# Kernel optimization log

Hardware: AMD Instinct MI355X
Metric: run time of the kernel (lower is better)

The kernel has to match this reference:

```python
import jax, jax.numpy as jnp
import numpy as np

B, P, M = 16, 16384, 2048
D_Z, D_PHI, D_R = 512, 256, 64
H1, H2 = 96, 96
IN_DIM = D_Z + 3 * D_PHI + D_R  # 1344


def setup_inputs() -> dict:
    key = jax.random.key(0)
    ks = jax.random.split(key, 8)
    g_q = jax.random.normal(ks[0], (B, D_Z), dtype=jnp.float32)
    Phi = jax.random.normal(ks[1], (M, D_PHI), dtype=jnp.float32)
    # pair indices with i < j (sort each row)
    pi = jax.random.randint(ks[2], (P, 2), 0, M, dtype=jnp.int64)
    pair_index = jnp.sort(pi, axis=-1)
    relation_features = jax.random.normal(ks[3], (P, D_R), dtype=jnp.float32)
    # learned MLP params (Linear weights stored [in, out])
    W1 = jax.random.normal(ks[4], (IN_DIM, H1), dtype=jnp.float32) / np.sqrt(IN_DIM)
    b1 = jnp.zeros((H1,), dtype=jnp.float32)
    W2 = jax.random.normal(ks[5], (H1, H2), dtype=jnp.float32) / np.sqrt(H1)
    b2 = jnp.zeros((H2,), dtype=jnp.float32)
    W3 = jax.random.normal(ks[6], (H2, 1), dtype=jnp.float32) / np.sqrt(H2)
    b3 = jnp.zeros((1,), dtype=jnp.float32)
    return {"g_q": g_q, "Phi": Phi, "pair_index": pair_index,
            "relation_features": relation_features,
            "W1": W1, "b1": b1, "W2": W2, "b2": b2, "W3": W3, "b3": b3}


def reference(g_q, Phi, pair_index, relation_features, W1, b1, W2, b2, W3, b3):
    # gather pair embeddings: [P, d_phi]
    phi_i = Phi[pair_index[:, 0]]
    phi_j = Phi[pair_index[:, 1]]
    # symmetric combine -> [P, 3*d_phi + d_r]
    pair_feats = jnp.concatenate(
        [phi_i + phi_j, jnp.abs(phi_i - phi_j), phi_i * phi_j, relation_features],
        axis=-1)
    b, p = g_q.shape[0], pair_feats.shape[0]
    # broadcast-concat -> x: [B, P, in_dim]
    x = jnp.concatenate(
        [jnp.broadcast_to(g_q[:, None, :], (b, p, g_q.shape[-1])),
         jnp.broadcast_to(pair_feats[None, :, :], (b, p, pair_feats.shape[-1]))],
        axis=-1)
    # small MLP: Linear -> GELU (erf, dropout is identity at eval) x2, then Linear(->1)
    h = jax.nn.gelu(x @ W1 + b1, approximate=False)
    h = jax.nn.gelu(h @ W2 + b2, approximate=False)
    out = h @ W3 + b3  # [B, P, 1]
    return out[..., 0]  # [B, P]
```

## Files before the change

### kernel.cpp

```cpp
#include <hip/hip_runtime.h>
#include <hip/hip_bf16.h>
#include <stdint.h>

static constexpr int P_N   = 16384;
static constexpr int D_Z   = 512;
static constexpr int D_PHI = 256;
static constexpr int D_R   = 64;
static constexpr int H     = 96;
static constexpr int KP    = 832;

using f32x4 = __attribute__((ext_vector_type(4))) float;
using s16x8 = __attribute__((ext_vector_type(8))) short;

__device__ __forceinline__ unsigned short f2bf(float f) {
    union { float f; uint32_t u; } v; v.f = f;
    return (unsigned short)((v.u + 0x7FFFu + ((v.u >> 16) & 1u)) >> 16);
}

__device__ __forceinline__ uint32_t pkbf2(float lo, float hi) {
    union { __hip_bfloat162 h; uint32_t u; } c;
    c.h = __float22bfloat162_rn(make_float2(lo, hi));
    return c.u;
}

__device__ __forceinline__ float gelu_f(float x) {
    float x2 = x * x;
    float u  = __builtin_fmaf(-0.1029444f, x2, -2.3022126f);
    float e  = __builtin_amdgcn_exp2f(x * u);
    return x * __builtin_amdgcn_rcpf(1.0f + e);
}

__global__ __launch_bounds__(256) void prep_kernel(
    const float* __restrict__ g_q, const float* __restrict__ W1,
    const float* __restrict__ b1, const float* __restrict__ W2,
    float* __restrict__ gqfrag, unsigned short* __restrict__ W1frag,
    unsigned short* __restrict__ W2frag)
{
    __shared__ float gql[D_Z];
    __shared__ float red[192];
    const int blk = blockIdx.x;
    const int t = threadIdx.x;
    if (blk < 16) {
        const int b = blk;
        for (int i = t; i < D_Z; i += 256) gql[i] = g_q[b * D_Z + i];
        __syncthreads();
        float acc = 0.f;
        if (t < 192) {
            const int n = t % 96, s = t / 96;
            const int k0 = s * 256;
            #pragma unroll 8
            for (int k = 0; k < 256; ++k)
                acc += gql[k0 + k] * W1[(k0 + k) * H + n];
            red[t] = acc;
        }
        __syncthreads();
        if (t < 96) {
            const float v = red[t] + red[t + 96] + b1[t];
            const int dst = ((t >> 5) * 64 + ((t >> 3) & 3) * 16 + b) * 8 + (t & 7);
            gqfrag[dst] = v;
        }
    } else if (blk < 328) {
        const int e = (blk - 16) * 256 + t;
        const int n = e / KP, k = e % KP;
        const int nf = n >> 4, lr = n & 15;
        const int kc = k >> 5, l4 = (k >> 3) & 3, ke = k & 7;
        W1frag[((nf * 26 + kc) * 64 + l4 * 16 + lr) * 8 + ke] =
            f2bf(W1[(D_Z + k) * H + n]);
    } else {
        const int e = (blk - 328) * 256 + t;
        const int n = e / H, k = e % H;
        const int nf = n >> 4, lr = n & 15;
        const int ks = k >> 5, l4 = (k >> 3) & 3, ke = k & 7;
        W2frag[((nf * 3 + ks) * 64 + l4 * 16 + lr) * 8 + ke] =
            f2bf(W2[k * H + n]);
    }
}

__global__ __launch_bounds__(512, 2) void fused9_kernel(
    const float* __restrict__ Phi, const int* __restrict__ pidx,
    const float* __restrict__ rel, const unsigned short* __restrict__ W1frag,
    const float* __restrict__ gqfrag, const unsigned short* __restrict__ W2frag,
    const float* __restrict__ b2, const float* __restrict__ W3,
    const float* __restrict__ b3, float* __restrict__ out)
{
    constexpr int FS = 840;
    __shared__ __align__(16) unsigned short feats[16 * FS];
    __shared__ __align__(16) float y1part[4][16][100];
    const int t = threadIdx.x;
    const int p0 = blockIdx.x * 16;

    for (int task = t; task < 1664; task += 512) {
        const int pair = task / 104;
        const int k = (task - pair * 104) * 8;
        float f[8];
        if (k < 768) {
            const int2 ij = *(const int2*)(pidx + 2 * (p0 + pair));
            const int kb = k & 255;
            const float* PI = Phi + (long)ij.x * D_PHI + kb;
            const float* PJ = Phi + (long)ij.y * D_PHI + kb;
            float4 a0 = *(const float4*)PI, a1 = *(const float4*)(PI + 4);
            float4 c0 = *(const float4*)PJ, c1 = *(const float4*)(PJ + 4);
            if (k < 256) {
                f[0]=a0.x+c0.x; f[1]=a0.y+c0.y; f[2]=a0.z+c0.z; f[3]=a0.w+c0.w;
                f[4]=a1.x+c1.x; f[5]=a1.y+c1.y; f[6]=a1.z+c1.z; f[7]=a1.w+c1.w;
            } else if (k < 512) {
                f[0]=fabsf(a0.x-c0.x); f[1]=fabsf(a0.y-c0.y); f[2]=fabsf(a0.z-c0.z); f[3]=fabsf(a0.w-c0.w);
                f[4]=fabsf(a1.x-c1.x); f[5]=fabsf(a1.y-c1.y); f[6]=fabsf(a1.z-c1.z); f[7]=fabsf(a1.w-c1.w);
            } else {
                f[0]=a0.x*c0.x; f[1]=a0.y*c0.y; f[2]=a0.z*c0.z; f[3]=a0.w*c0.w;
                f[4]=a1.x*c1.x; f[5]=a1.y*c1.y; f[6]=a1.z*c1.z; f[7]=a1.w*c1.w;
            }
        } else {
            const float* R = rel + (long)(p0 + pair) * D_R + (k - 768);
            float4 a0 = *(const float4*)R, a1 = *(const float4*)(R + 4);
            f[0]=a0.x; f[1]=a0.y; f[2]=a0.z; f[3]=a0.w;
            f[4]=a1.x; f[5]=a1.y; f[6]=a1.z; f[7]=a1.w;
        }
        uint4 pk;
        pk.x = pkbf2(f[0], f[1]);
        pk.y = pkbf2(f[2], f[3]);
        pk.z = pkbf2(f[4], f[5]);
        pk.w = pkbf2(f[6], f[7]);
        *(uint4*)&feats[pair * FS + k] = pk;
    }
    __syncthreads();

    const int w  = t >> 6;
    const int l  = t & 63;
    const int lr = l & 15, l4 = l >> 4;

    {
        const int kq = w & 3, ng = w >> 2;
        const int kc_lo = (kq < 2) ? kq * 7 : 14 + (kq - 2) * 6;
        const int kc_hi = (kq < 2) ? kc_lo + 7 : kc_lo + 6;
        f32x4 acc[3];
        acc[0] = (f32x4){0.f,0.f,0.f,0.f};
        acc[1] = (f32x4){0.f,0.f,0.f,0.f};
        acc[2] = (f32x4){0.f,0.f,0.f,0.f};
        const unsigned short* Arow = &feats[lr * FS + l4 * 8];
        for (int kc = kc_lo; kc < kc_hi; ++kc) {
            const s16x8 a = *(const s16x8*)(Arow + kc * 32);
            #pragma unroll
            for (int j = 0; j < 3; ++j) {
                const s16x8 bb = *(const s16x8*)(W1frag +
                    (((ng * 3 + j) * 26 + kc) * 64 + l) * 8);
                acc[j] = __builtin_amdgcn_mfma_f32_16x16x32_bf16(a, bb, acc[j], 0, 0, 0);
            }
        }
        #pragma unroll
        for (int j = 0; j < 3; ++j)
            #pragma unroll
            for (int r = 0; r < 4; ++r)
                y1part[kq][l4 * 4 + r][ng * 48 + j * 16 + lr] = acc[j][r];
    }
    __syncthreads();

    float part[2][4];
    #pragma unroll
    for (int mf = 0; mf < 2; ++mf) {
        const int pl = 2 * w + mf;

        s16x8 afr[3];
        #pragma unroll
        for (int ks = 0; ks < 3; ++ks) {
            const int c = ks * 32 + l4 * 8;
            const float* gp = gqfrag + (ks * 64 + l) * 8;
            float4 g0 = *(const float4*)gp, g1 = *(const float4*)(gp + 4);
            float s0x=g0.x, s0y=g0.y, s0z=g0.z, s0w=g0.w;
            float s1x=g1.x, s1y=g1.y, s1z=g1.z, s1w=g1.w;
            #pragma unroll
            for (int kq = 0; kq < 4; ++kq) {
                const float* yp = &y1part[kq][pl][c];
                float4 u0 = *(const float4*)yp, u1 = *(const float4*)(yp + 4);
                s0x += u0.x; s0y += u0.y; s0z += u0.z; s0w += u0.w;
                s1x += u1.x; s1y += u1.y; s1z += u1.z; s1w += u1.w;
            }
            union { s16x8 v; uint32_t u[4]; } pk;
            pk.u[0] = pkbf2(gelu_f(s0x), gelu_f(s0y));
            pk.u[1] = pkbf2(gelu_f(s0z), gelu_f(s0w));
            pk.u[2] = pkbf2(gelu_f(s1x), gelu_f(s1y));
            pk.u[3] = pkbf2(gelu_f(s1z), gelu_f(s1w));
            afr[ks] = pk.v;
        }

        f32x4 acc2[6];
        #pragma unroll
        for (int nf = 0; nf < 6; ++nf) {
            const float bv = b2[nf * 16 + lr];
            acc2[nf] = (f32x4){bv, bv, bv, bv};
        }
        #pragma unroll
        for (int ks = 0; ks < 3; ++ks) {
            #pragma unroll
            for (int nf = 0; nf < 6; ++nf) {
                const s16x8 bb = *(const s16x8*)(W2frag + ((nf * 3 + ks) * 64 + l) * 8);
                acc2[nf] = __builtin_amdgcn_mfma_f32_16x16x32_bf16(afr[ks], bb, acc2[nf], 0, 0, 0);
            }
        }

        part[mf][0] = part[mf][1] = part[mf][2] = part[mf][3] = 0.f;
        #pragma unroll
        for (int nf = 0; nf < 6; ++nf) {
            const float wv = W3[nf * 16 + lr];
            #pragma unroll
            for (int r4 = 0; r4 < 4; ++r4)
                part[mf][r4] = __builtin_fmaf(gelu_f(acc2[nf][r4]), wv, part[mf][r4]);
        }
    }

    #pragma unroll
    for (int mask = 1; mask <= 8; mask <<= 1)
        #pragma unroll
        for (int mf = 0; mf < 2; ++mf)
            #pragma unroll
            for (int r4 = 0; r4 < 4; ++r4)
                part[mf][r4] += __shfl_xor(part[mf][r4], mask, 64);
    if (lr == 0) {
        const float b3v = b3[0];
        #pragma unroll
        for (int mf = 0; mf < 2; ++mf)
            #pragma unroll
            for (int r4 = 0; r4 < 4; ++r4)
                out[(l4 * 4 + r4) * P_N + p0 + 2 * w + mf] = part[mf][r4] + b3v;
    }
}

extern "C" void kernel_launch(void* const* d_in, const int* in_sizes, int n_in,
                              void* d_out, int out_size, void* d_ws, size_t ws_size,
                              hipStream_t stream)
{
    const float* g_q  = (const float*)d_in[0];
    const float* Phi  = (const float*)d_in[1];
    const int*   pidx = (const int*)d_in[2];
    const float* rel  = (const float*)d_in[3];
    const float* W1   = (const float*)d_in[4];
    const float* b1   = (const float*)d_in[5];
    const float* W2   = (const float*)d_in[6];
    const float* b2   = (const float*)d_in[7];
    const float* W3   = (const float*)d_in[8];
    const float* b3   = (const float*)d_in[9];
    float* out = (float*)d_out;

    char* ws = (char*)d_ws;
    float*          gqfrag = (float*)(ws + 0);
    unsigned short* W1frag = (unsigned short*)(ws + 8192);
    unsigned short* W2frag = (unsigned short*)(ws + 167936);

    hipLaunchKernelGGL(prep_kernel, dim3(364), dim3(256), 0, stream,
                       g_q, W1, b1, W2, gqfrag, W1frag, W2frag);
    hipLaunchKernelGGL(fused9_kernel, dim3(P_N / 16), dim3(512), 0, stream,
                       Phi, pidx, rel, W1frag, gqfrag, W2frag, b2, W3, b3, out);
}
```

Measured before the change: 44.06 us.

## Restructure pair-feature gather and split layer-1 K into two halves

Each thread now loads one 8-wide slice of Phi_i and Phi_j once and writes the sum, absolute-difference and product features from the same registers. Previously the two rows were reloaded three times across the task loop. The layer-1 MFMA work is repartitioned so six waves each cover 2 N-fragments over half of K, instead of eight waves each covering 3 N-fragments over a quarter of K. This halves the y1part partial buffers and the cross-wave reduction reads, but leaves two waves idle during layer 1.

```diff
diff --git a/kernel.cpp b/kernel.cpp
--- a/kernel.cpp
+++ b/kernel.cpp
@@ -76,7 +76,7 @@
     }
 }
 
-__global__ __launch_bounds__(512, 2) void fused9_kernel(
+__global__ __launch_bounds__(512, 2) void fused11_kernel(
     const float* __restrict__ Phi, const int* __restrict__ pidx,
     const float* __restrict__ rel, const unsigned short* __restrict__ W1frag,
     const float* __restrict__ gqfrag, const unsigned short* __restrict__ W2frag,
@@ -85,43 +85,42 @@
 {
     constexpr int FS = 840;
     __shared__ __align__(16) unsigned short feats[16 * FS];
-    __shared__ __align__(16) float y1part[4][16][100];
+    __shared__ __align__(16) float y1part[2][16][100];
     const int t = threadIdx.x;
     const int p0 = blockIdx.x * 16;
 
-    for (int task = t; task < 1664; task += 512) {
-        const int pair = task / 104;
-        const int k = (task - pair * 104) * 8;
-        float f[8];
-        if (k < 768) {
-            const int2 ij = *(const int2*)(pidx + 2 * (p0 + pair));
-            const int kb = k & 255;
-            const float* PI = Phi + (long)ij.x * D_PHI + kb;
-            const float* PJ = Phi + (long)ij.y * D_PHI + kb;
-            float4 a0 = *(const float4*)PI, a1 = *(const float4*)(PI + 4);
-            float4 c0 = *(const float4*)PJ, c1 = *(const float4*)(PJ + 4);
-            if (k < 256) {
-                f[0]=a0.x+c0.x; f[1]=a0.y+c0.y; f[2]=a0.z+c0.z; f[3]=a0.w+c0.w;
-                f[4]=a1.x+c1.x; f[5]=a1.y+c1.y; f[6]=a1.z+c1.z; f[7]=a1.w+c1.w;
-            } else if (k < 512) {
-                f[0]=fabsf(a0.x-c0.x); f[1]=fabsf(a0.y-c0.y); f[2]=fabsf(a0.z-c0.z); f[3]=fabsf(a0.w-c0.w);
-                f[4]=fabsf(a1.x-c1.x); f[5]=fabsf(a1.y-c1.y); f[6]=fabsf(a1.z-c1.z); f[7]=fabsf(a1.w-c1.w);
-            } else {
-                f[0]=a0.x*c0.x; f[1]=a0.y*c0.y; f[2]=a0.z*c0.z; f[3]=a0.w*c0.w;
-                f[4]=a1.x*c1.x; f[5]=a1.y*c1.y; f[6]=a1.z*c1.z; f[7]=a1.w*c1.w;
-            }
-        } else {
-            const float* R = rel + (long)(p0 + pair) * D_R + (k - 768);
-            float4 a0 = *(const float4*)R, a1 = *(const float4*)(R + 4);
-            f[0]=a0.x; f[1]=a0.y; f[2]=a0.z; f[3]=a0.w;
-            f[4]=a1.x; f[5]=a1.y; f[6]=a1.z; f[7]=a1.w;
-        }
-        uint4 pk;
-        pk.x = pkbf2(f[0], f[1]);
-        pk.y = pkbf2(f[2], f[3]);
-        pk.z = pkbf2(f[4], f[5]);
-        pk.w = pkbf2(f[6], f[7]);
-        *(uint4*)&feats[pair * FS + k] = pk;
+    {
+        const int p = t >> 5, c = t & 31, kb = c * 8;
+        const int2 ij = *(const int2*)(pidx + 2 * (p0 + p));
+        const float* PI = Phi + (long)ij.x * D_PHI + kb;
+        const float* PJ = Phi + (long)ij.y * D_PHI + kb;
+        float4 a0 = *(const float4*)PI, a1 = *(const float4*)(PI + 4);
+        float4 c0 = *(const float4*)PJ, c1 = *(const float4*)(PJ + 4);
+        uint4 s, d, q;
+        s.x = pkbf2(a0.x + c0.x, a0.y + c0.y);
+        s.y = pkbf2(a0.z + c0.z, a0.w + c0.w);
+        s.z = pkbf2(a1.x + c1.x, a1.y + c1.y);
+        s.w = pkbf2(a1.z + c1.z, a1.w + c1.w);
+        d.x = pkbf2(fabsf(a0.x - c0.x), fabsf(a0.y - c0.y));
+        d.y = pkbf2(fabsf(a0.z - c0.z), fabsf(a0.w - c0.w));
+        d.z = pkbf2(fabsf(a1.x - c1.x), fabsf(a1.y - c1.y));
+        d.w = pkbf2(fabsf(a1.z - c1.z), fabsf(a1.w - c1.w));
+        q.x = pkbf2(a0.x * c0.x, a0.y * c0.y);
+        q.y = pkbf2(a0.z * c0.z, a0.w * c0.w);
+        q.z = pkbf2(a1.x * c1.x, a1.y * c1.y);
+        q.w = pkbf2(a1.z * c1.z, a1.w * c1.w);
+        *(uint4*)&feats[p * FS + kb]       = s;
+        *(uint4*)&feats[p * FS + 256 + kb] = d;
+        *(uint4*)&feats[p * FS + 512 + kb] = q;
+        if (t < 128) {
+            const int p2 = t >> 3, c2 = t & 7;
+            const float* R = rel + (long)(p0 + p2) * D_R + c2 * 8;
+            float4 r0 = *(const float4*)R, r1 = *(const float4*)(R + 4);
+            uint4 rr;
+            rr.x = pkbf2(r0.x, r0.y); rr.y = pkbf2(r0.z, r0.w);
+            rr.z = pkbf2(r1.x, r1.y); rr.w = pkbf2(r1.z, r1.w);
+            *(uint4*)&feats[p2 * FS + 768 + c2 * 8] = rr;
+        }
     }
     __syncthreads();
 
@@ -129,29 +128,27 @@
     const int l  = t & 63;
     const int lr = l & 15, l4 = l >> 4;
 
-    {
-        const int kq = w & 3, ng = w >> 2;
-        const int kc_lo = (kq < 2) ? kq * 7 : 14 + (kq - 2) * 6;
-        const int kc_hi = (kq < 2) ? kc_lo + 7 : kc_lo + 6;
-        f32x4 acc[3];
+    if (w < 6) {
+        const int kh = w & 1, ng = w >> 1;
+        const int kc0 = kh * 13;
+        f32x4 acc[2];
         acc[0] = (f32x4){0.f,0.f,0.f,0.f};
         acc[1] = (f32x4){0.f,0.f,0.f,0.f};
-        acc[2] = (f32x4){0.f,0.f,0.f,0.f};
         const unsigned short* Arow = &feats[lr * FS + l4 * 8];
-        for (int kc = kc_lo; kc < kc_hi; ++kc) {
+        for (int kc = kc0; kc < kc0 + 13; ++kc) {
             const s16x8 a = *(const s16x8*)(Arow + kc * 32);
             #pragma unroll
-            for (int j = 0; j < 3; ++j) {
+            for (int j = 0; j < 2; ++j) {
                 const s16x8 bb = *(const s16x8*)(W1frag +
-                    (((ng * 3 + j) * 26 + kc) * 64 + l) * 8);
+                    (((ng * 2 + j) * 26 + kc) * 64 + l) * 8);
                 acc[j] = __builtin_amdgcn_mfma_f32_16x16x32_bf16(a, bb, acc[j], 0, 0, 0);
             }
         }
         #pragma unroll
-        for (int j = 0; j < 3; ++j)
+        for (int j = 0; j < 2; ++j)
             #pragma unroll
             for (int r = 0; r < 4; ++r)
-                y1part[kq][l4 * 4 + r][ng * 48 + j * 16 + lr] = acc[j][r];
+                y1part[kh][l4 * 4 + r][ng * 32 + j * 16 + lr] = acc[j][r];
     }
     __syncthreads();
 
@@ -166,20 +163,15 @@
             const int c = ks * 32 + l4 * 8;
             const float* gp = gqfrag + (ks * 64 + l) * 8;
             float4 g0 = *(const float4*)gp, g1 = *(const float4*)(gp + 4);
-            float s0x=g0.x, s0y=g0.y, s0z=g0.z, s0w=g0.w;
-            float s1x=g1.x, s1y=g1.y, s1z=g1.z, s1w=g1.w;
-            #pragma unroll
-            for (int kq = 0; kq < 4; ++kq) {
-                const float* yp = &y1part[kq][pl][c];
-                float4 u0 = *(const float4*)yp, u1 = *(const float4*)(yp + 4);
-                s0x += u0.x; s0y += u0.y; s0z += u0.z; s0w += u0.w;
-                s1x += u1.x; s1y += u1.y; s1z += u1.z; s1w += u1.w;
-            }
+            const float* ya = &y1part[0][pl][c];
+            const float* yb = &y1part[1][pl][c];
+            float4 u0 = *(const float4*)ya, u1 = *(const float4*)(ya + 4);
+            float4 v0 = *(const float4*)yb, v1 = *(const float4*)(yb + 4);
             union { s16x8 v; uint32_t u[4]; } pk;
-            pk.u[0] = pkbf2(gelu_f(s0x), gelu_f(s0y));
-            pk.u[1] = pkbf2(gelu_f(s0z), gelu_f(s0w));
-            pk.u[2] = pkbf2(gelu_f(s1x), gelu_f(s1y));
-            pk.u[3] = pkbf2(gelu_f(s1z), gelu_f(s1w));
+            pk.u[0] = pkbf2(gelu_f(g0.x + u0.x + v0.x), gelu_f(g0.y + u0.y + v0.y));
+            pk.u[1] = pkbf2(gelu_f(g0.z + u0.z + v0.z), gelu_f(g0.w + u0.w + v0.w));
+            pk.u[2] = pkbf2(gelu_f(g1.x + u1.x + v1.x), gelu_f(g1.y + u1.y + v1.y));
+            pk.u[3] = pkbf2(gelu_f(g1.z + u1.z + v1.z), gelu_f(g1.w + u1.w + v1.w));
             afr[ks] = pk.v;
         }
 
@@ -248,6 +240,6 @@
 
     hipLaunchKernelGGL(prep_kernel, dim3(364), dim3(256), 0, stream,
                        g_q, W1, b1, W2, gqfrag, W1frag, W2frag);
-    hipLaunchKernelGGL(fused9_kernel, dim3(P_N / 16), dim3(512), 0, stream,
+    hipLaunchKernelGGL(fused11_kernel, dim3(P_N / 16), dim3(512), 0, stream,
                        Phi, pidx, rel, W1frag, gqfrag, W2frag, b2, W3, b3, out);
 }
```

Result: faster. 42.92 us (-2.6%).
